# Performance work log

Measured on AMD Instinct MI355X. Metric: run time of the kernel, lower is better.

The kernel has to match this reference:

```python
import jax, jax.numpy as jnp
import numpy as np

B, CIN, COUT, K, H, W = 16, 256, 256, 3, 64, 64
COND = 512


def setup_inputs() -> dict:
    key = jax.random.key(0)
    ks = jax.random.split(key, 10)
    X = jax.random.normal(ks[0], (B, CIN, H, W), dtype=jnp.float32)
    cond_v = jax.random.normal(ks[1], (B, COND), dtype=jnp.float32)
    # conv weight [O, I, kh, kw]
    conv_w = jax.random.normal(ks[2], (COUT, CIN, K, K), dtype=jnp.float32) / np.sqrt(CIN * K * K)
    w0 = jax.random.normal(ks[3], (COND, COND), dtype=jnp.float32) / np.sqrt(COND)
    b0 = jnp.zeros((COND,), dtype=jnp.float32)
    w1 = jax.random.normal(ks[4], (COND, COND), dtype=jnp.float32) / np.sqrt(COND)
    b1 = jnp.zeros((COND,), dtype=jnp.float32)
    w_out = jax.random.normal(ks[5], (CIN, COND), dtype=jnp.float32) / np.sqrt(COND)
    b_out = jnp.zeros((CIN,), dtype=jnp.float32)
    return {"X": X, "cond_v": cond_v, "conv_w": conv_w,
            "w0": w0, "b0": b0, "w1": w1, "b1": b1,
            "w_out": w_out, "b_out": b_out}


def reference(X, cond_v, conv_w, w0, b0, w1, b1, w_out, b_out):
    # proj_cond MLP: (Linear+SiLU) x depth, final Linear -> in_channels
    h = jax.nn.silu(cond_v @ w0.T + b0)
    h = jax.nn.silu(h @ w1.T + b1)
    scale = h @ w_out.T + b_out + 1.0          # [B, I]
    # modulate: bw[b,o,i,kh,kw] = w[o,i,kh,kw] * scale[b,i]
    bw = conv_w[None] * scale[:, None, :, None, None]
    # demodulate across (i, kh, kw)
    demod = jax.lax.rsqrt(jnp.sum(bw * bw, axis=(2, 3, 4)) + 1e-8)  # [B, O]
    bw = bw * demod[:, :, None, None, None]
    b, o, i, kh, kw = bw.shape
    # per-sample conv via grouped conv: x -> [1, B*I, H, W], w -> [B*O, I, kh, kw]
    x = X.reshape(1, b * i, X.shape[2], X.shape[3])
    w = bw.reshape(b * o, i, kh, kw)
    out = jax.lax.conv_general_dilated(
        x, w, window_strides=(1, 1), padding="SAME",
        feature_group_count=b,
        dimension_numbers=("NCHW", "OIHW", "NCHW"))
    return out.reshape(b, o, out.shape[2], out.shape[3])
```

## Files before the change

kernel.cpp:

```cpp
#include <hip/hip_runtime.h>
#include <hip/hip_bf16.h>
#include <cstdint>

#define NB 16
#define CI 256
#define CO 256
#define HH 64
#define WW 64
#define CC 512
#define HP 66
#define WP 66

typedef short short8 __attribute__((ext_vector_type(8)));
typedef float floatx4 __attribute__((ext_vector_type(4)));
typedef unsigned int uintx4 __attribute__((ext_vector_type(4)));

__device__ __forceinline__ void g2lds16(const void* g, void* l) {
  __builtin_amdgcn_global_load_lds((const __attribute__((address_space(1))) void*)g,
                                   (__attribute__((address_space(3))) void*)l, 16, 0, 0);
}

#define ASM_VMCNT0() do { asm volatile("s_waitcnt vmcnt(0)" ::: "memory"); \
                          __builtin_amdgcn_sched_barrier(0); } while (0)
#define ASM_VMCNT2() do { asm volatile("s_waitcnt vmcnt(2)" ::: "memory"); \
                          __builtin_amdgcn_sched_barrier(0); } while (0)
#define ASM_VMCNT3() do { asm volatile("s_waitcnt vmcnt(3)" ::: "memory"); \
                          __builtin_amdgcn_sched_barrier(0); } while (0)
#define RAW_BAR() do { __builtin_amdgcn_sched_barrier(0);  \
                       __builtin_amdgcn_s_barrier();       \
                       __builtin_amdgcn_sched_barrier(0); } while (0)

template<int KD, int N, bool SILU, bool PLUSONE, int BJ>
__global__ void k_mlp(const float* __restrict__ in, const float* __restrict__ w,
                      const float* __restrict__ bias, float* __restrict__ out) {
  __shared__ float4 sin4[KD / 4];
  const int nb = N / BJ;
  int b = blockIdx.x / nb;
  int j = (blockIdx.x % nb) * BJ + threadIdx.x;
  const float4* in4 = reinterpret_cast<const float4*>(in + (size_t)b * KD);
  for (int k = threadIdx.x; k < KD / 4; k += BJ) sin4[k] = in4[k];
  __syncthreads();
  float acc = bias[j];
  const float4* wr = reinterpret_cast<const float4*>(w + (size_t)j * KD);
#pragma unroll 8
  for (int kk = 0; kk < KD / 4; ++kk) {
    float4 wv = wr[kk];
    float4 sv = sin4[kk];
    acc += wv.x * sv.x + wv.y * sv.y + wv.z * sv.z + wv.w * sv.w;
  }
  if (SILU) acc = acc / (1.0f + __expf(-acc));
  if (PLUSONE) acc += 1.0f;
  out[(size_t)b * N + j] = acc;
}

__global__ void k_repack(const float* __restrict__ cw, __hip_bfloat16* __restrict__ Wt,
                         float* __restrict__ wsq) {
  int gid = blockIdx.x * 256 + threadIdx.x;
  if (gid >= CO * CI) return;
  const float* p = cw + (size_t)gid * 9;
  float s = 0.0f;
#pragma unroll
  for (int t = 0; t < 9; ++t) {
    float v = p[t];
    s += v * v;
    Wt[(size_t)t * CO * CI + gid] = __float2bfloat16(v);
  }
  wsq[gid] = s;
}

__global__ void k_demod(const float* __restrict__ wsq, const float* __restrict__ scale,
                        float* __restrict__ demod) {
  __shared__ float s2[CI];
  int b = blockIdx.x;
  int o = threadIdx.x;
  float sv = scale[b * CI + o];
  s2[o] = sv * sv;
  __syncthreads();
  float acc = 0.0f;
  const float4* wr = reinterpret_cast<const float4*>(wsq + (size_t)o * CI);
  const float4* s4 = reinterpret_cast<const float4*>(s2);
#pragma unroll 8
  for (int i = 0; i < CI / 4; ++i) {
    float4 wv = wr[i];
    float4 sq = s4[i];
    acc += wv.x * sq.x + wv.y * sq.y + wv.z * sq.z + wv.w * sq.w;
  }
  demod[b * CO + o] = rsqrtf(acc + 1e-8f);
}

__global__ void k_scalex(const float* __restrict__ X, const float* __restrict__ scale,
                         __hip_bfloat16* __restrict__ Xs) {
  __shared__ float tile[64][68];
  __shared__ float ssc[64];
  int bid = blockIdx.x;
  int b = bid >> 8;
  int rem = bid & 255;
  int h = rem >> 2;
  int i0 = (rem & 3) * 64;
  int t = threadIdx.x;
  if (t < 64) ssc[t] = scale[b * CI + i0 + t];

  __hip_bfloat16* xs_img = Xs + (size_t)b * HP * WP * CI;
  uintx4 z = {0u, 0u, 0u, 0u};
  if (t < 16) {
    int px = (t >> 3) * 65;
    int sl = t & 7;
    *reinterpret_cast<uintx4*>(xs_img + (((size_t)(h + 1)) * WP + px) * CI + i0 + sl * 8) = z;
  }
  if (h == 0) {
    for (int u = t; u < 66 * 8; u += 256) {
      int px = u >> 3, sl = u & 7;
      *reinterpret_cast<uintx4*>(xs_img + ((size_t)px) * CI + i0 + sl * 8) = z;
    }
  }
  if (h == 63) {
    for (int u = t; u < 66 * 8; u += 256) {
      int px = u >> 3, sl = u & 7;
      *reinterpret_cast<uintx4*>(xs_img + ((size_t)65 * WP + px) * CI + i0 + sl * 8) = z;
    }
  }

  const float* src = X + (((size_t)b * CI + i0) * HH + h) * WW;
  int ii_base = t >> 4;
  int w4 = (t & 15) * 4;
#pragma unroll
  for (int r2 = 0; r2 < 4; ++r2) {
    int ii = r2 * 16 + ii_base;
    int key = ((ii >> 3) & 7) << 2;
    *reinterpret_cast<float4*>(&tile[ii][w4 ^ key]) =
        *reinterpret_cast<const float4*>(src + (size_t)ii * HH * WW + w4);
  }
  __syncthreads();
  int u = t & 7;
  int wl = t >> 3;
  int key = u << 2;
#pragma unroll
  for (int iter = 0; iter < 2; ++iter) {
    int w2 = wl + iter * 32;
    union { unsigned short us[8]; uintx4 v; } pk;
#pragma unroll
    for (int j = 0; j < 8; ++j) {
      int ii = u * 8 + j;
      float v = tile[ii][w2 ^ key] * ssc[ii];
      __hip_bfloat16 hb = __float2bfloat16(v);
      pk.us[j] = *reinterpret_cast<unsigned short*>(&hb);
    }
    *reinterpret_cast<uintx4*>(xs_img + (((size_t)(h + 1)) * WP + (w2 + 1)) * CI + i0 + u * 8) = pk.v;
  }
}

__global__ __launch_bounds__(256, 2)
void k_conv(const __hip_bfloat16* __restrict__ Xs, const __hip_bfloat16* __restrict__ Wt,
            const float* __restrict__ demod, float* __restrict__ out) {
  __shared__ __align__(16) char lds[2 * 28672 + 3 * 8192];
  char* sX0 = lds;
  char* sA0 = lds + 57344;

  int wg = (blockIdx.x & 7) * 64 + (blockIdx.x >> 3);
  int b = wg >> 5;
  int rem = wg & 31;
  int ht = rem >> 1;
  int ob = rem & 1;
  int h0 = ht * 4;
  int o0 = ob * 128;

  int tid = threadIdx.x;
  int wv = tid >> 6;
  int lane = tid & 63;
  int lhi = lane >> 4;
  int llo = lane & 15;
  int wo2 = wv >> 1;
  int wpx = wv & 1;

  floatx4 acc[4][8];
#pragma unroll
  for (int m = 0; m < 4; ++m)
#pragma unroll
    for (int n = 0; n < 8; ++n) acc[m][n] = (floatx4){0.f, 0.f, 0.f, 0.f};

  const __hip_bfloat16* xs_img = Xs + (size_t)b * HP * WP * CI;

  int xoff[7];
#pragma unroll
  for (int s = 0; s < 7; ++s) {
    int j = wv + 4 * s;
    int pr = 16 * j + (lane >> 2);
    int prc = pr > 431 ? 431 : pr;
    int lr = prc / 72;
    int wp = prc - lr * 72;
    if (wp > 65) wp = 65;
    int ksl = (lane & 3) ^ ((pr >> 1) & 3);
    xoff[s] = ((h0 + lr) * WP + wp) * CI + ksl * 8;
  }
  int a_off[2];
#pragma unroll
  for (int jj = 0; jj < 2; ++jj) {
    int ol = 32 * wv + 16 * jj + (lane >> 2);
    int sl = (lane & 3) ^ ((ol >> 1) & 3);
    a_off[jj] = (o0 + ol) * CI + sl * 8;
  }

  int row_a[4], key_a[4];
#pragma unroll
  for (int m = 0; m < 4; ++m) {
    row_a[m] = wo2 * 64 + m * 16 + llo;
    key_a[m] = (row_a[m] >> 1) & 3;
  }

#pragma unroll
  for (int s = 0; s < 7; ++s)
    g2lds16(xs_img + xoff[s], sX0 + (wv + 4 * s) * 1024);
#pragma unroll
  for (int jj = 0; jj < 2; ++jj)
    g2lds16(Wt + a_off[jj], sA0 + (wv * 2 + jj) * 1024);
  ASM_VMCNT0();
  RAW_BAR();

  for (int c = 0; c < 8; ++c) {
    const char* xbuf = sX0 + (c & 1) * 28672;
#pragma unroll
    for (int t = 0; t < 9; ++t) {
      int gt = c * 9 + t;
      bool xiss = (t >= 2) && (c < 7);
      if (xiss) {
        int s = t - 2;
        g2lds16(xs_img + xoff[s] + (c + 1) * 32,
                sX0 + ((c + 1) & 1) * 28672 + (wv + 4 * s) * 1024);
      }
      if (gt < 71) {
        int nt = (t == 8) ? 0 : t + 1;
        int ncc = (t == 8) ? c + 1 : c;
        const __hip_bfloat16* wb = Wt + (size_t)nt * CO * CI + ncc * 32;
        char* ad = sA0 + ((t + 1) % 3) * 8192;
        g2lds16(wb + a_off[0], ad + (wv * 2 + 0) * 1024);
        g2lds16(wb + a_off[1], ad + (wv * 2 + 1) * 1024);
        if (xiss) { ASM_VMCNT3(); } else { ASM_VMCNT2(); }
      } else {
        ASM_VMCNT0();
      }
      RAW_BAR();

      __builtin_amdgcn_s_setprio(1);
      const char* sA = sA0 + (t % 3) * 8192;
      int kh = t / 3;
      int kw = t - kh * 3;
      short8 af[4];
#pragma unroll
      for (int m = 0; m < 4; ++m)
        af[m] = *reinterpret_cast<const short8*>(sA + row_a[m] * 64 + ((lhi ^ key_a[m]) << 4));
#pragma unroll
      for (int n = 0; n < 8; ++n) {
        int stripe = wpx * 2 + (n >> 2) + kh;
        int px = (n & 3) * 16 + llo + kw;
        int prl = stripe * 72 + px;
        short8 bq = *reinterpret_cast<const short8*>(
            xbuf + prl * 64 + ((lhi ^ ((prl >> 1) & 3)) << 4));
#pragma unroll
        for (int m = 0; m < 4; ++m)
          acc[m][n] = __builtin_amdgcn_mfma_f32_16x16x32_bf16(af[m], bq, acc[m][n], 0, 0, 0);
      }
      __builtin_amdgcn_s_setprio(0);
    }
  }

#pragma unroll
  for (int m = 0; m < 4; ++m) {
    int obase_o = o0 + wo2 * 64 + m * 16 + lhi * 4;
    float4 dmv = *reinterpret_cast<const float4*>(demod + (size_t)b * CO + obase_o);
#pragma unroll
    for (int j = 0; j < 4; ++j) {
      int o = obase_o + j;
      float dm = (j == 0) ? dmv.x : (j == 1) ? dmv.y : (j == 2) ? dmv.z : dmv.w;
      float* orow = out + (((size_t)b * CO + o) * HH + h0) * WW;
#pragma unroll
      for (int n = 0; n < 8; ++n) {
        int row = wpx * 2 + (n >> 2);
        int col = (n & 3) * 16 + llo;
        orow[(size_t)row * WW + col] = acc[m][n][j] * dm;
      }
    }
  }
}

extern "C" void kernel_launch(void* const* d_in, const int* in_sizes, int n_in,
                              void* d_out, int out_size, void* d_ws, size_t ws_size,
                              hipStream_t stream) {
  const float* X      = (const float*)d_in[0];
  const float* cond_v = (const float*)d_in[1];
  const float* conv_w = (const float*)d_in[2];
  const float* w0     = (const float*)d_in[3];
  const float* b0     = (const float*)d_in[4];
  const float* w1     = (const float*)d_in[5];
  const float* b1     = (const float*)d_in[6];
  const float* w_out  = (const float*)d_in[7];
  const float* b_out  = (const float*)d_in[8];
  float* out = (float*)d_out;

  char* ws = (char*)d_ws;
  const size_t XS_BYTES  = (size_t)NB * HP * WP * CI * 2;
  const size_t WT_BYTES  = (size_t)9 * CO * CI * 2;
  const size_t WSQ_BYTES = (size_t)CO * CI * 4;
  __hip_bfloat16* Xs = (__hip_bfloat16*)ws;
  __hip_bfloat16* Wt = (__hip_bfloat16*)(ws + XS_BYTES);
  float* wsq   = (float*)(ws + XS_BYTES + WT_BYTES);
  float* h0b   = (float*)(ws + XS_BYTES + WT_BYTES + WSQ_BYTES);
  float* h1b   = h0b + NB * CC;
  float* scale = h1b + NB * CC;
  float* demod = scale + NB * CI;

  k_repack<<<(CO * CI) / 256, 256, 0, stream>>>(conv_w, Wt, wsq);
  k_mlp<CC, CC, true, false, 128><<<NB * (CC / 128), 128, 0, stream>>>(cond_v, w0, b0, h0b);
  k_mlp<CC, CC, true, false, 128><<<NB * (CC / 128), 128, 0, stream>>>(h0b, w1, b1, h1b);
  k_mlp<CC, CI, false, true, 128><<<NB * (CI / 128), 128, 0, stream>>>(h1b, w_out, b_out, scale);
  k_demod<<<NB, CO, 0, stream>>>(wsq, scale, demod);
  k_scalex<<<NB * 64 * 4, 256, 0, stream>>>(X, scale, Xs);
  k_conv<<<NB * 32, 256, 0, stream>>>(Xs, Wt, demod, out);
}
```

Measured before the change: 131.4 us.

## Load conv weights directly into registers in MFMA fragment layout, drop weight LDS staging

The repack kernel now writes weights in a layout that matches the MFMA A-fragment, so each lane in the conv kernel loads its weight fragments straight from global memory with 16-byte reads instead of staging them through a triple-buffered LDS ring. Barriers and waitcounts drop from once per tap to once per channel chunk, and the B-fragments are read from LDS into registers before the MFMA loop. This cuts LDS use and synchronisation, but weight fetches now come from L2/global memory with no explicit prefetch, so their latency may be exposed on every tap.

```diff
diff --git a/kernel.cpp b/kernel.cpp
--- a/kernel.cpp
+++ b/kernel.cpp
@@ -20,11 +20,8 @@
                                    (__attribute__((address_space(3))) void*)l, 16, 0, 0);
 }
 
-#define ASM_VMCNT0() do { asm volatile("s_waitcnt vmcnt(0)" ::: "memory"); \
-                          __builtin_amdgcn_sched_barrier(0); } while (0)
-#define ASM_VMCNT2() do { asm volatile("s_waitcnt vmcnt(2)" ::: "memory"); \
-                          __builtin_amdgcn_sched_barrier(0); } while (0)
-#define ASM_VMCNT3() do { asm volatile("s_waitcnt vmcnt(3)" ::: "memory"); \
+#define ASM_VMCNT0() do { __builtin_amdgcn_sched_barrier(0);               \
+                          asm volatile("s_waitcnt vmcnt(0)" ::: "memory"); \
                           __builtin_amdgcn_sched_barrier(0); } while (0)
 #define RAW_BAR() do { __builtin_amdgcn_sched_barrier(0);  \
                        __builtin_amdgcn_s_barrier();       \
@@ -53,17 +50,20 @@
   out[(size_t)b * N + j] = acc;
 }
 
-__global__ void k_repack(const float* __restrict__ cw, __hip_bfloat16* __restrict__ Wt,
+__global__ void k_repack(const float* __restrict__ cw, __hip_bfloat16* __restrict__ Wt2,
                          float* __restrict__ wsq) {
   int gid = blockIdx.x * 256 + threadIdx.x;
   if (gid >= CO * CI) return;
+  int o = gid >> 8;
+  int i = gid & 255;
+  int base_i = ((i >> 5) * 4 + ((i >> 3) & 3)) * 2048 + o * 8 + (i & 7);
   const float* p = cw + (size_t)gid * 9;
   float s = 0.0f;
 #pragma unroll
   for (int t = 0; t < 9; ++t) {
     float v = p[t];
     s += v * v;
-    Wt[(size_t)t * CO * CI + gid] = __float2bfloat16(v);
+    Wt2[(size_t)t * 65536 + base_i] = __float2bfloat16(v);
   }
   wsq[gid] = s;
 }
@@ -150,11 +150,10 @@
 }
 
 __global__ __launch_bounds__(256, 2)
-void k_conv(const __hip_bfloat16* __restrict__ Xs, const __hip_bfloat16* __restrict__ Wt,
+void k_conv(const __hip_bfloat16* __restrict__ Xs, const __hip_bfloat16* __restrict__ Wt2,
             const float* __restrict__ demod, float* __restrict__ out) {
-  __shared__ __align__(16) char lds[2 * 28672 + 3 * 8192];
+  __shared__ __align__(16) char lds[2 * 28672];
   char* sX0 = lds;
-  char* sA0 = lds + 57344;
 
   int wg = (blockIdx.x & 7) * 64 + (blockIdx.x >> 3);
   int b = wg >> 5;
@@ -192,27 +191,14 @@
     int ksl = (lane & 3) ^ ((pr >> 1) & 3);
     xoff[s] = ((h0 + lr) * WP + wp) * CI + ksl * 8;
   }
-  int a_off[2];
-#pragma unroll
-  for (int jj = 0; jj < 2; ++jj) {
-    int ol = 32 * wv + 16 * jj + (lane >> 2);
-    int sl = (lane & 3) ^ ((ol >> 1) & 3);
-    a_off[jj] = (o0 + ol) * CI + sl * 8;
-  }
-
-  int row_a[4], key_a[4];
-#pragma unroll
-  for (int m = 0; m < 4; ++m) {
-    row_a[m] = wo2 * 64 + m * 16 + llo;
-    key_a[m] = (row_a[m] >> 1) & 3;
-  }
+  int aofs[4];
+#pragma unroll
+  for (int m = 0; m < 4; ++m)
+    aofs[m] = lhi * 2048 + (o0 + wo2 * 64 + m * 16 + llo) * 8;
 
 #pragma unroll
   for (int s = 0; s < 7; ++s)
     g2lds16(xs_img + xoff[s], sX0 + (wv + 4 * s) * 1024);
-#pragma unroll
-  for (int jj = 0; jj < 2; ++jj)
-    g2lds16(Wt + a_off[jj], sA0 + (wv * 2 + jj) * 1024);
   ASM_VMCNT0();
   RAW_BAR();
 
@@ -220,47 +206,35 @@
     const char* xbuf = sX0 + (c & 1) * 28672;
 #pragma unroll
     for (int t = 0; t < 9; ++t) {
-      int gt = c * 9 + t;
-      bool xiss = (t >= 2) && (c < 7);
-      if (xiss) {
-        int s = t - 2;
-        g2lds16(xs_img + xoff[s] + (c + 1) * 32,
-                sX0 + ((c + 1) & 1) * 28672 + (wv + 4 * s) * 1024);
-      }
-      if (gt < 71) {
-        int nt = (t == 8) ? 0 : t + 1;
-        int ncc = (t == 8) ? c + 1 : c;
-        const __hip_bfloat16* wb = Wt + (size_t)nt * CO * CI + ncc * 32;
-        char* ad = sA0 + ((t + 1) % 3) * 8192;
-        g2lds16(wb + a_off[0], ad + (wv * 2 + 0) * 1024);
-        g2lds16(wb + a_off[1], ad + (wv * 2 + 1) * 1024);
-        if (xiss) { ASM_VMCNT3(); } else { ASM_VMCNT2(); }
-      } else {
-        ASM_VMCNT0();
-      }
-      RAW_BAR();
-
-      __builtin_amdgcn_s_setprio(1);
-      const char* sA = sA0 + (t % 3) * 8192;
+      const __hip_bfloat16* wb = Wt2 + (size_t)(t * 8 + c) * 8192;
+      short8 af[4];
+#pragma unroll
+      for (int m = 0; m < 4; ++m)
+        af[m] = *reinterpret_cast<const short8*>(wb + aofs[m]);
+      if (t <= 6 && c < 7)
+        g2lds16(xs_img + xoff[t] + (c + 1) * 32,
+                sX0 + ((c + 1) & 1) * 28672 + (wv + 4 * t) * 1024);
       int kh = t / 3;
       int kw = t - kh * 3;
-      short8 af[4];
-#pragma unroll
-      for (int m = 0; m < 4; ++m)
-        af[m] = *reinterpret_cast<const short8*>(sA + row_a[m] * 64 + ((lhi ^ key_a[m]) << 4));
+      short8 bq[8];
 #pragma unroll
       for (int n = 0; n < 8; ++n) {
         int stripe = wpx * 2 + (n >> 2) + kh;
         int px = (n & 3) * 16 + llo + kw;
         int prl = stripe * 72 + px;
-        short8 bq = *reinterpret_cast<const short8*>(
+        bq[n] = *reinterpret_cast<const short8*>(
             xbuf + prl * 64 + ((lhi ^ ((prl >> 1) & 3)) << 4));
+      }
+      __builtin_amdgcn_s_setprio(1);
+#pragma unroll
+      for (int n = 0; n < 8; ++n)
 #pragma unroll
         for (int m = 0; m < 4; ++m)
-          acc[m][n] = __builtin_amdgcn_mfma_f32_16x16x32_bf16(af[m], bq, acc[m][n], 0, 0, 0);
-      }
+          acc[m][n] = __builtin_amdgcn_mfma_f32_16x16x32_bf16(af[m], bq[n], acc[m][n], 0, 0, 0);
       __builtin_amdgcn_s_setprio(0);
     }
+    ASM_VMCNT0();
+    if (c < 7) RAW_BAR();
   }
 
 #pragma unroll
@@ -298,21 +272,21 @@
 
   char* ws = (char*)d_ws;
   const size_t XS_BYTES  = (size_t)NB * HP * WP * CI * 2;
-  const size_t WT_BYTES  = (size_t)9 * CO * CI * 2;
+  const size_t WT_BYTES  = (size_t)9 * 65536 * 2;
   const size_t WSQ_BYTES = (size_t)CO * CI * 4;
-  __hip_bfloat16* Xs = (__hip_bfloat16*)ws;
-  __hip_bfloat16* Wt = (__hip_bfloat16*)(ws + XS_BYTES);
+  __hip_bfloat16* Xs  = (__hip_bfloat16*)ws;
+  __hip_bfloat16* Wt2 = (__hip_bfloat16*)(ws + XS_BYTES);
   float* wsq   = (float*)(ws + XS_BYTES + WT_BYTES);
   float* h0b   = (float*)(ws + XS_BYTES + WT_BYTES + WSQ_BYTES);
   float* h1b   = h0b + NB * CC;
   float* scale = h1b + NB * CC;
   float* demod = scale + NB * CI;
 
-  k_repack<<<(CO * CI) / 256, 256, 0, stream>>>(conv_w, Wt, wsq);
+  k_repack<<<(CO * CI) / 256, 256, 0, stream>>>(conv_w, Wt2, wsq);
   k_mlp<CC, CC, true, false, 128><<<NB * (CC / 128), 128, 0, stream>>>(cond_v, w0, b0, h0b);
   k_mlp<CC, CC, true, false, 128><<<NB * (CC / 128), 128, 0, stream>>>(h0b, w1, b1, h1b);
   k_mlp<CC, CI, false, true, 128><<<NB * (CI / 128), 128, 0, stream>>>(h1b, w_out, b_out, scale);
   k_demod<<<NB, CO, 0, stream>>>(wsq, scale, demod);
   k_scalex<<<NB * 64 * 4, 256, 0, stream>>>(X, scale, Xs);
-  k_conv<<<NB * 32, 256, 0, stream>>>(Xs, Wt, demod, out);
-}
+  k_conv<<<NB * 32, 256, 0, stream>>>(Xs, Wt2, demod, out);
+}
```

Result: slower. 144.5 us (+10.0%).
